# Kernel tuning notes

Hardware: AMD Instinct MI355X
Metric: run time of the kernel (lower is better)

## Reference

```python
import jax, jax.numpy as jnp
import numpy as np

D_MODEL = 1024
N_HEADS = 16
HEAD_DIM = D_MODEL // N_HEADS
SEQ_LEN = 2048
D_FF = 4 * D_MODEL
LCC_SCALE = 0.1
LN_EPS = 1e-5
NORM_EPS = 1e-12  # F.normalize eps


def _layer_norm(x, g, b):
    mu = jnp.mean(x, axis=-1, keepdims=True)
    var = jnp.mean(jnp.square(x - mu), axis=-1, keepdims=True)
    return (x - mu) * jax.lax.rsqrt(var + LN_EPS) * g + b


def setup_inputs() -> dict:
    key = jax.random.key(0)
    ks = jax.random.split(key, 8)
    s = 0.02  # weight init scale
    return {
        "x": jax.random.normal(ks[0], (SEQ_LEN, D_MODEL), jnp.float32),
        "lcc_values": jax.random.uniform(ks[1], (SEQ_LEN,), jnp.float32),
        "w_qkv": jax.random.normal(ks[2], (D_MODEL, 3 * D_MODEL), jnp.float32) * s,
        "b_qkv": jnp.zeros((3 * D_MODEL,), jnp.float32),
        "w_out": jax.random.normal(ks[3], (D_MODEL, D_MODEL), jnp.float32) * s,
        "b_out": jnp.zeros((D_MODEL,), jnp.float32),
        "ln1_g": jnp.ones((D_MODEL,), jnp.float32),
        "ln1_b": jnp.zeros((D_MODEL,), jnp.float32),
        "ln2_g": jnp.ones((D_MODEL,), jnp.float32),
        "ln2_b": jnp.zeros((D_MODEL,), jnp.float32),
        "w_ff1": jax.random.normal(ks[4], (D_MODEL, D_FF), jnp.float32) * s,
        "b_ff1": jnp.zeros((D_FF,), jnp.float32),
        "w_ff2": jax.random.normal(ks[5], (D_FF, D_MODEL), jnp.float32) * s,
        "b_ff2": jnp.zeros((D_MODEL,), jnp.float32),
    }


def reference(x, lcc_values, w_qkv, b_qkv, w_out, b_out, ln1_g, ln1_b,
              ln2_g, ln2_b, w_ff1, b_ff1, w_ff2, b_ff2):
    L = x.shape[0]
    scaling = HEAD_DIM ** -0.5

    normed = _layer_norm(x, ln1_g, ln1_b)
    qkv = normed @ w_qkv + b_qkv                      # [L, 3D]
    qkv = qkv.reshape(L, 3, N_HEADS, HEAD_DIM)
    q = jnp.transpose(qkv[:, 0], (1, 0, 2))           # [H, L, d]
    k = jnp.transpose(qkv[:, 1], (1, 0, 2))
    v = jnp.transpose(qkv[:, 2], (1, 0, 2))

    # cosine attention: L2-normalize q, k
    q = q / jnp.maximum(jnp.linalg.norm(q, axis=-1, keepdims=True), NORM_EPS)
    k = k / jnp.maximum(jnp.linalg.norm(k, axis=-1, keepdims=True), NORM_EPS)
    q = q * scaling

    scores = jnp.einsum('hld,hmd->hlm', q, k)         # [H, L, L]
    bias = (lcc_values[:, None] + lcc_values[None, :]) * 0.5 * LCC_SCALE
    scores = jnp.clip(scores + bias[None], -10.0, 10.0)
    probs = jax.nn.softmax(scores, axis=-1)

    attn = jnp.einsum('hlm,hmd->hld', probs, v)       # [H, L, d]
    attn = jnp.transpose(attn, (1, 0, 2)).reshape(L, D_MODEL)
    x = x + (attn @ w_out + b_out)

    normed2 = _layer_norm(x, ln2_g, ln2_b)
    h = jax.nn.gelu(normed2 @ w_ff1 + b_ff1, approximate=False)
    x = x + (h @ w_ff2 + b_ff2)
    return x
```

## Files before the change

### kernel.cpp

```cpp
#include <hip/hip_runtime.h>
#include <hip/hip_bf16.h>

#define D_MODEL 1024
#define SEQ 2048
#define NH 16
#define HD 64
#define DFF 4096

typedef __attribute__((ext_vector_type(8))) __bf16 bf16x8;
typedef __attribute__((ext_vector_type(4))) float f32x4;

__device__ __forceinline__ unsigned short f2bf(float f) {
    union { float f; unsigned u; } v; v.f = f;
    unsigned r = v.u + 0x7fffu + ((v.u >> 16) & 1u);
    return (unsigned short)(r >> 16);
}
__device__ __forceinline__ unsigned pack2(float a, float b) {
    return (unsigned)f2bf(a) | ((unsigned)f2bf(b) << 16);
}
__device__ __forceinline__ float bf2f(unsigned short u) {
    union { unsigned u; float f; } v; v.u = ((unsigned)u) << 16;
    return v.f;
}
__device__ __forceinline__ bf16x8 ld_frag(const unsigned short* p) {
    union { uint4 u; bf16x8 b; } c;
    c.u = *(const uint4*)p;
    return c.b;
}

typedef __attribute__((address_space(3))) unsigned lds_u32;
typedef const __attribute__((address_space(1))) unsigned glob_u32;
__device__ __forceinline__ void gl_lds16(const unsigned short* g, unsigned short* l) {
    __builtin_amdgcn_global_load_lds((glob_u32*)g, (lds_u32*)l, 16, 0, 0);
}

#define MFMA16(a,b,c) __builtin_amdgcn_mfma_f32_16x16x32_bf16(a,b,c,0,0,0)

__global__ __launch_bounds__(256) void wcast_all(const float* __restrict__ wq, const float* __restrict__ wo,
                                                 const float* __restrict__ wf1, const float* __restrict__ wf2,
                                                 unsigned short* __restrict__ oq, unsigned short* __restrict__ oo,
                                                 unsigned short* __restrict__ of1, unsigned short* __restrict__ of2) {
    __shared__ unsigned short lt[64][72];
    int id = blockIdx.x;
    const float* W; unsigned short* O; int K, N, nb, kb;
    if (id < 768)       { W = wq;  O = oq;  K = 1024; N = 3072; nb = id % 48; kb = id / 48; }
    else if (id < 1024) { id -= 768;  W = wo;  O = oo;  K = 1024; N = 1024; nb = id & 15; kb = id >> 4; }
    else if (id < 2048) { id -= 1024; W = wf1; O = of1; K = 1024; N = 4096; nb = id & 63; kb = id >> 6; }
    else                { id -= 2048; W = wf2; O = of2; K = 4096; N = 1024; nb = id & 15; kb = id >> 4; }
    int t = threadIdx.x;
    int r = t >> 2, c0 = (t & 3) << 4;
    const float* src = W + (size_t)(kb*64 + r) * N + nb*64 + c0;
    float4 f0 = ((const float4*)src)[0];
    float4 f1 = ((const float4*)src)[1];
    float4 f2 = ((const float4*)src)[2];
    float4 f3 = ((const float4*)src)[3];
    unsigned* dst = (unsigned*)&lt[r][c0];
    dst[0]=pack2(f0.x,f0.y); dst[1]=pack2(f0.z,f0.w);
    dst[2]=pack2(f1.x,f1.y); dst[3]=pack2(f1.z,f1.w);
    dst[4]=pack2(f2.x,f2.y); dst[5]=pack2(f2.z,f2.w);
    dst[6]=pack2(f3.x,f3.y); dst[7]=pack2(f3.z,f3.w);
    __syncthreads();
    int n_ = t >> 2, k0 = (t & 3) << 4;
    unsigned obuf[8];
#pragma unroll
    for (int i = 0; i < 8; i++)
        obuf[i] = (unsigned)lt[k0 + 2*i][n_] | ((unsigned)lt[k0 + 2*i + 1][n_] << 16);
    unsigned short* out = O + (size_t)(nb*64 + n_) * K + kb*64 + k0;
    ((uint4*)out)[0] = *(uint4*)&obuf[0];
    ((uint4*)out)[1] = *(uint4*)&obuf[4];
}

__global__ __launch_bounds__(256) void ln_kernel(const float* __restrict__ x,
                                                 const float* __restrict__ g,
                                                 const float* __restrict__ b,
                                                 unsigned short* __restrict__ out) {
    int row = blockIdx.x, t = threadIdx.x;
    float4 v = ((const float4*)(x + (size_t)row * D_MODEL))[t];
    float s  = v.x + v.y + v.z + v.w;
    float sq = v.x*v.x + v.y*v.y + v.z*v.z + v.w*v.w;
#pragma unroll
    for (int m = 1; m < 64; m <<= 1) { s += __shfl_xor(s, m, 64); sq += __shfl_xor(sq, m, 64); }
    __shared__ float ls[4], lq[4];
    int wave = t >> 6, lane = t & 63;
    if (lane == 0) { ls[wave] = s; lq[wave] = sq; }
    __syncthreads();
    s  = ls[0]+ls[1]+ls[2]+ls[3];
    sq = lq[0]+lq[1]+lq[2]+lq[3];
    float mu  = s * (1.0f / D_MODEL);
    float var = sq * (1.0f / D_MODEL) - mu * mu;
    float rs  = rsqrtf(var + 1e-5f);
    int c = t * 4;
    float y0 = (v.x - mu) * rs * g[c+0] + b[c+0];
    float y1 = (v.y - mu) * rs * g[c+1] + b[c+1];
    float y2 = (v.z - mu) * rs * g[c+2] + b[c+2];
    float y3 = (v.w - mu) * rs * g[c+3] + b[c+3];
    unsigned* o = (unsigned*)(out + (size_t)row * D_MODEL + c);
    o[0] = pack2(y0, y1); o[1] = pack2(y2, y3);
}

__global__ __launch_bounds__(256) void reduce_ln(const float* __restrict__ x,
                                                 const float* __restrict__ bout,
                                                 const unsigned short* __restrict__ parts,
                                                 const float* __restrict__ g,
                                                 const float* __restrict__ b,
                                                 float* __restrict__ x1,
                                                 unsigned short* __restrict__ x2n) {
    int row = blockIdx.x, t = threadIdx.x;
    int i = row * 256 + t;
    float4 v = ((const float4*)x)[i];
    float4 bb = ((const float4*)bout)[t];
    v.x += bb.x; v.y += bb.y; v.z += bb.z; v.w += bb.w;
    ushort4 u0 = ((const ushort4*)parts)[i];
    ushort4 u1 = ((const ushort4*)(parts + (size_t)SEQ*D_MODEL))[i];
    v.x += bf2f(u0.x) + bf2f(u1.x);
    v.y += bf2f(u0.y) + bf2f(u1.y);
    v.z += bf2f(u0.z) + bf2f(u1.z);
    v.w += bf2f(u0.w) + bf2f(u1.w);
    ((float4*)x1)[i] = v;
    float s  = v.x + v.y + v.z + v.w;
    float sq = v.x*v.x + v.y*v.y + v.z*v.z + v.w*v.w;
#pragma unroll
    for (int m = 1; m < 64; m <<= 1) { s += __shfl_xor(s, m, 64); sq += __shfl_xor(sq, m, 64); }
    __shared__ float ls[4], lq[4];
    int wave = t >> 6, lane = t & 63;
    if (lane == 0) { ls[wave] = s; lq[wave] = sq; }
    __syncthreads();
    s  = ls[0]+ls[1]+ls[2]+ls[3];
    sq = lq[0]+lq[1]+lq[2]+lq[3];
    float mu  = s * (1.0f / D_MODEL);
    float var = sq * (1.0f / D_MODEL) - mu * mu;
    float rs  = rsqrtf(var + 1e-5f);
    int c = t * 4;
    float y0 = (v.x - mu) * rs * g[c+0] + b[c+0];
    float y1 = (v.y - mu) * rs * g[c+1] + b[c+1];
    float y2 = (v.z - mu) * rs * g[c+2] + b[c+2];
    float y3 = (v.w - mu) * rs * g[c+3] + b[c+3];
    unsigned* o = (unsigned*)(x2n + (size_t)row * D_MODEL + c);
    o[0] = pack2(y0, y1); o[1] = pack2(y2, y3);
}

__global__ __launch_bounds__(256) void reduce_ff2(const float* __restrict__ res,
                                                  const float* __restrict__ bias,
                                                  const unsigned short* __restrict__ parts,
                                                  float* __restrict__ out) {
    int i = blockIdx.x * 256 + threadIdx.x;
    float4 r = ((const float4*)res)[i];
    float4 b = ((const float4*)bias)[i & (D_MODEL/4 - 1)];
    r.x += b.x; r.y += b.y; r.z += b.z; r.w += b.w;
#pragma unroll
    for (int p = 0; p < 4; p++) {
        ushort4 u = ((const ushort4*)(parts + (size_t)p * SEQ * D_MODEL))[i];
        r.x += bf2f(u.x); r.y += bf2f(u.y); r.z += bf2f(u.z); r.w += bf2f(u.w);
    }
    ((float4*)out)[i] = r;
}

#define TMg 128
#define TNg 64
#define SMEM_U16 (2 * (TMg + TNg) * 64)
__device__ __forceinline__ void gemm_core(const unsigned short* __restrict__ A,
                                          const unsigned short* __restrict__ Bt,
                                          int K, int K0, int KS, int bm, int bn,
                                          unsigned short* smem, f32x4 acc[4][2],
                                          int wave, int lane) {
    constexpr int AI = 4, BI = 2, MI = 4, NI = 2;
    constexpr int HALF = (TMg + TNg) * 64;
    int quad = lane >> 4, lr = lane & 15;

    const unsigned short* pa[AI];
    int aoff[AI];
#pragma unroll
    for (int i = 0; i < AI; i++) {
        int rl = wave*32 + i*8 + (lane >> 3);
        int ss = (lane & 7) ^ (rl & 7);
        pa[i] = A + (size_t)(bm*TMg + rl) * K + K0 + ss*8;
        aoff[i] = (wave*32 + i*8) * 64;
    }
    const unsigned short* pb[BI];
    int boff[BI];
#pragma unroll
    for (int i = 0; i < BI; i++) {
        int rl = wave*16 + i*8 + (lane >> 3);
        int ss = (lane & 7) ^ (rl & 7);
        pb[i] = Bt + (size_t)(bn*TNg + rl) * K + K0 + ss*8;
        boff[i] = TMg*64 + (wave*16 + i*8) * 64;
    }

    int wr = (wave >> 1) * 64, wc = (wave & 1) * 32;
    int foA[2][MI], foB[2][NI];
#pragma unroll
    for (int i = 0; i < MI; i++) {
        int row = wr + i*16 + lr;
        foA[0][i] = row*64 + ((quad     ^ (row & 7)))*8;
        foA[1][i] = row*64 + (((quad+4) ^ (row & 7)))*8;
    }
#pragma unroll
    for (int j = 0; j < NI; j++) {
        int row = wc + j*16 + lr;
        foB[0][j] = TMg*64 + row*64 + ((quad     ^ (row & 7)))*8;
        foB[1][j] = TMg*64 + row*64 + (((quad+4) ^ (row & 7)))*8;
    }

#pragma unroll
    for (int i = 0; i < AI; i++) gl_lds16(pa[i], smem + aoff[i]);
#pragma unroll
    for (int i = 0; i < BI; i++) gl_lds16(pb[i], smem + boff[i]);

    int bo = 0;
    for (int kk = 0; kk < KS; kk += 64) {
        __syncthreads();
        if (kk + 64 < KS) {
            int nb = bo ^ HALF;
#pragma unroll
            for (int i = 0; i < AI; i++) gl_lds16(pa[i] + kk + 64, smem + nb + aoff[i]);
#pragma unroll
            for (int i = 0; i < BI; i++) gl_lds16(pb[i] + kk + 64, smem + nb + boff[i]);
        }
#pragma unroll
        for (int h = 0; h < 2; h++) {
            bf16x8 af[MI], bfr[NI];
#pragma unroll
            for (int i = 0; i < MI; i++) af[i]  = ld_frag(smem + bo + foA[h][i]);
#pragma unroll
            for (int j = 0; j < NI; j++) bfr[j] = ld_frag(smem + bo + foB[h][j]);
#pragma unroll
            for (int i = 0; i < MI; i++)
#pragma unroll
                for (int j = 0; j < NI; j++)
                    acc[i][j] = MFMA16(af[i], bfr[j], acc[i][j]);
        }
        bo ^= HALF;
    }
}

__device__ __forceinline__ void acc_init(f32x4 acc[4][2]) {
    f32x4 z = {0.f, 0.f, 0.f, 0.f};
#pragma unroll
    for (int i = 0; i < 4; i++) { acc[i][0] = z; acc[i][1] = z; }
}

__global__ __launch_bounds__(256) void k_gemm_qkv(const unsigned short* __restrict__ A,
                                                  const unsigned short* __restrict__ Bt,
                                                  const float* __restrict__ bias,
                                                  unsigned short* __restrict__ qn,
                                                  unsigned short* __restrict__ kn,
                                                  unsigned short* __restrict__ vt) {
    __shared__ unsigned short smem[SMEM_U16];
    int t = threadIdx.x;
    int bn = blockIdx.x, bm = blockIdx.y;
    int wave = t >> 6, lane = t & 63;
    int quad = lane >> 4, lr = lane & 15;
    f32x4 acc[4][2];
    acc_init(acc);
    gemm_core(A, Bt, 1024, 0, 1024, bm, bn, smem, acc, wave, lane);

    int wr = (wave >> 1) * 64, wc = (wave & 1) * 32;
    int sec = bn >> 4, h = bn & 15;
    float bv0 = bias[bn*64 + wc + lr];
    float bv1 = bias[bn*64 + wc + 16 + lr];
#pragma unroll
    for (int i = 0; i < 4; i++)
#pragma unroll
        for (int r = 0; r < 4; r++) { acc[i][0][r] += bv0; acc[i][1][r] += bv1; }

    if (sec < 2) {
        float* sums = (float*)smem;
        __syncthreads();
#pragma unroll
        for (int i = 0; i < 4; i++)
#pragma unroll
            for (int r = 0; r < 4; r++) {
                float s = acc[i][0][r]*acc[i][0][r] + acc[i][1][r]*acc[i][1][r];
                s += __shfl_xor(s, 1, 64); s += __shfl_xor(s, 2, 64);
                s += __shfl_xor(s, 4, 64); s += __shfl_xor(s, 8, 64);
                if (lr == 0) sums[(wr + i*16 + quad*4 + r)*2 + (wave & 1)] = s;
            }
        __syncthreads();
        unsigned short* dst = (sec == 0) ? qn : kn;
        float mul = (sec == 0) ? 0.125f : 1.0f;
#pragma unroll
        for (int i = 0; i < 4; i++)
#pragma unroll
            for (int r = 0; r < 4; r++) {
                int row = wr + i*16 + quad*4 + r;
                float tot = sums[row*2] + sums[row*2 + 1];
                float scale = mul / fmaxf(sqrtf(tot), 1e-12f);
                size_t base = ((size_t)h*SEQ + bm*128 + row) * HD;
                dst[base + wc + lr]      = f2bf(acc[i][0][r] * scale);
                dst[base + wc + 16 + lr] = f2bf(acc[i][1][r] * scale);
            }
    } else {
        __syncthreads();
        unsigned short (*lv)[130] = (unsigned short (*)[130])smem;
#pragma unroll
        for (int i = 0; i < 4; i++)
#pragma unroll
            for (int j = 0; j < 2; j++)
#pragma unroll
                for (int r = 0; r < 4; r++)
                    lv[wc + j*16 + lr][wr + i*16 + quad*4 + r] = f2bf(acc[i][j][r]);
        __syncthreads();
        int d = t >> 2, l0 = (t & 3) * 32;
        unsigned short* ov = vt + ((size_t)(h*HD + d)) * SEQ + bm*128 + l0;
        ((uint4*)ov)[0] = *(uint4*)&lv[d][l0];
        ((uint4*)ov)[1] = *(uint4*)&lv[d][l0 + 8];
        ((uint4*)ov)[2] = *(uint4*)&lv[d][l0 + 16];
        ((uint4*)ov)[3] = *(uint4*)&lv[d][l0 + 24];
    }
}

template<int SPLITK>
__device__ __forceinline__ void gemm_part(const unsigned short* A, const unsigned short* Bt,
                                          unsigned short* C, int M, int N, int K) {
    __shared__ unsigned short smem[SMEM_U16];
    int t = threadIdx.x;
    int bn = blockIdx.x, bm = blockIdx.y, kz = blockIdx.z;
    int wave = t >> 6, lane = t & 63;
    int quad = lane >> 4, lr = lane & 15;
    int KS = K / SPLITK;
    f32x4 acc[4][2];
    acc_init(acc);
    gemm_core(A, Bt, K, kz*KS, KS, bm, bn, smem, acc, wave, lane);
    int wr = (wave >> 1) * 64, wc = (wave & 1) * 32;
    unsigned short* P = C + (size_t)kz * M * N;
#pragma unroll
    for (int i = 0; i < 4; i++)
#pragma unroll
        for (int j = 0; j < 2; j++) {
            int row0 = bm*TMg + wr + i*16 + quad*4;
            int col  = bn*TNg + wc + j*16 + lr;
#pragma unroll
            for (int r = 0; r < 4; r++)
                P[(size_t)(row0 + r) * N + col] = f2bf(acc[i][j][r]);
        }
}
__global__ __launch_bounds__(256) void k_gemm_op(const unsigned short* A, const unsigned short* Bt,
                                                 unsigned short* C, int M, int N, int K) {
    gemm_part<2>(A, Bt, C, M, N, K);
}
__global__ __launch_bounds__(256) void k_gemm_ff2(const unsigned short* A, const unsigned short* Bt,
                                                  unsigned short* C, int M, int N, int K) {
    gemm_part<4>(A, Bt, C, M, N, K);
}

__global__ __launch_bounds__(256) void k_gemm_ff1(const unsigned short* __restrict__ A,
                                                  const unsigned short* __restrict__ Bt,
                                                  const float* __restrict__ bias,
                                                  unsigned short* __restrict__ C,
                                                  int M, int N, int K) {
    __shared__ unsigned short smem[SMEM_U16];
    int t = threadIdx.x;
    int bn = blockIdx.x, bm = blockIdx.y;
    int wave = t >> 6, lane = t & 63;
    int quad = lane >> 4, lr = lane & 15;
    f32x4 acc[4][2];
    acc_init(acc);
    gemm_core(A, Bt, K, 0, K, bm, bn, smem, acc, wave, lane);
    int wr = (wave >> 1) * 64, wc = (wave & 1) * 32;
#pragma unroll
    for (int i = 0; i < 4; i++)
#pragma unroll
        for (int j = 0; j < 2; j++) {
            int row0 = bm*TMg + wr + i*16 + quad*4;
            int col  = bn*TNg + wc + j*16 + lr;
            float bv = bias[col];
#pragma unroll
            for (int r = 0; r < 4; r++) {
                float v = acc[i][j][r] + bv;
                v = 0.5f * v * (1.0f + erff(v * 0.70710678118654752f));
                C[(size_t)(row0 + r) * N + col] = f2bf(v);
            }
        }
}

#define KSPLIT 2
#define KTILES (SEQ / 64 / KSPLIT)
__global__ __launch_bounds__(256) void attn_kernel(const unsigned short* __restrict__ qn,
                                                   const unsigned short* __restrict__ kn,
                                                   const unsigned short* __restrict__ vt,
                                                   const float* __restrict__ lcc,
                                                   float* __restrict__ num_ws,
                                                   float* __restrict__ den_ws) {
    __shared__ unsigned short lQ[64][72];
    __shared__ unsigned short lK[64][72];
    __shared__ unsigned short lV[64][72];
    __shared__ unsigned short lP[64][72];
    __shared__ float lL[SEQ / KSPLIT];
    int h = blockIdx.x, qb = blockIdx.y, kz = blockIdx.z;
    int t = threadIdx.x;
    int rl = t >> 2, c0 = (t & 3) << 4;
    const unsigned short* pq = qn + ((size_t)h*SEQ + qb*64 + rl)*HD + c0;
    *(uint4*)&lQ[rl][c0]     = ((const uint4*)pq)[0];
    *(uint4*)&lQ[rl][c0 + 8] = ((const uint4*)pq)[1];
    for (int i = t; i < SEQ/KSPLIT; i += 256) lL[i] = 0.05f * lcc[kz*(SEQ/KSPLIT) + i];
    __syncthreads();
    int wave = t >> 6, lane = t & 63, quad = lane >> 4, lr = lane & 15;
    float lqv[4];
#pragma unroll
    for (int r = 0; r < 4; r++) lqv[r] = 0.05f * lcc[qb*64 + wave*16 + quad*4 + r];
    bf16x8 aq0 = ld_frag(&lQ[wave*16 + lr][quad*8]);
    bf16x8 aq1 = ld_frag(&lQ[wave*16 + lr][32 + quad*8]);
    f32x4 z = {0.f, 0.f, 0.f, 0.f};
    f32x4 oacc[4]; oacc[0]=z; oacc[1]=z; oacc[2]=z; oacc[3]=z;
    float den[4] = {0.f, 0.f, 0.f, 0.f};

    const unsigned short* kn0 = kn + (size_t)h*SEQ*HD + (size_t)kz*(SEQ/KSPLIT)*HD;
    const unsigned short* vt0 = vt + (size_t)h*HD*SEQ + kz*(SEQ/KSPLIT);

    for (int kb = 0; kb < KTILES; kb++) {
        __syncthreads();
        const unsigned short* pk = kn0 + (size_t)(kb*64 + rl)*HD + c0;
        uint4 k0v = ((const uint4*)pk)[0], k1v = ((const uint4*)pk)[1];
        const unsigned short* pv = vt0 + (size_t)rl*SEQ + kb*64 + c0;
        uint4 v0v = ((const uint4*)pv)[0], v1v = ((const uint4*)pv)[1];
        *(uint4*)&lK[rl][c0]     = k0v; *(uint4*)&lK[rl][c0 + 8] = k1v;
        *(uint4*)&lV[rl][c0]     = v0v; *(uint4*)&lV[rl][c0 + 8] = v1v;
        __syncthreads();
#pragma unroll
        for (int j = 0; j < 4; j++) {
            bf16x8 b0 = ld_frag(&lK[j*16 + lr][quad*8]);
            bf16x8 b1 = ld_frag(&lK[j*16 + lr][32 + quad*8]);
            f32x4 s = z;
            s = MFMA16(aq0, b0, s);
            s = MFMA16(aq1, b1, s);
            float lm = lL[kb*64 + j*16 + lr];
#pragma unroll
            for (int r = 0; r < 4; r++) {
                float sv = s[r] + lqv[r] + lm;
                sv = fminf(fmaxf(sv, -10.f), 10.f);
                float p = __expf(sv);
                den[r] += p;
                lP[wave*16 + quad*4 + r][j*16 + lr] = f2bf(p);
            }
        }
        bf16x8 ap0 = ld_frag(&lP[wave*16 + lr][quad*8]);
        bf16x8 ap1 = ld_frag(&lP[wave*16 + lr][32 + quad*8]);
#pragma unroll
        for (int j2 = 0; j2 < 4; j2++) {
            bf16x8 b0 = ld_frag(&lV[j2*16 + lr][quad*8]);
            bf16x8 b1 = ld_frag(&lV[j2*16 + lr][32 + quad*8]);
            oacc[j2] = MFMA16(ap0, b0, oacc[j2]);
            oacc[j2] = MFMA16(ap1, b1, oacc[j2]);
        }
    }
#pragma unroll
    for (int r = 0; r < 4; r++)
#pragma unroll
        for (int m = 1; m < 16; m <<= 1) den[r] += __shfl_xor(den[r], m, 64);

    float* nump = num_ws + (((size_t)(h*32 + qb)) * KSPLIT + kz) * 4096;
#pragma unroll
    for (int j2 = 0; j2 < 4; j2++)
#pragma unroll
        for (int r = 0; r < 4; r++)
            nump[(wave*16 + quad*4 + r) * 64 + j2*16 + lr] = oacc[j2][r];
    if (lr == 0) {
        float* denp = den_ws + (((size_t)(h*32 + qb)) * KSPLIT + kz) * 64;
#pragma unroll
        for (int r = 0; r < 4; r++) denp[wave*16 + quad*4 + r] = den[r];
    }
}

__global__ __launch_bounds__(256) void attn_comb(const float* __restrict__ num_ws,
                                                 const float* __restrict__ den_ws,
                                                 unsigned short* __restrict__ attn) {
    int hq = blockIdx.x;
    int h = hq >> 5, qb = hq & 31;
    int t = threadIdx.x;
    int row = t >> 2, col0 = (t & 3) << 4;
    const float* n0 = num_ws + ((size_t)hq * KSPLIT) * 4096 + row*64 + col0;
    const float* n1 = n0 + 4096;
    float d = den_ws[(size_t)hq * KSPLIT * 64 + row] + den_ws[((size_t)hq * KSPLIT + 1) * 64 + row];
    float inv = 1.0f / d;
    unsigned ob[8];
#pragma unroll
    for (int i = 0; i < 4; i++) {
        float4 a = ((const float4*)n0)[i];
        float4 b = ((const float4*)n1)[i];
        ob[2*i]   = pack2((a.x + b.x) * inv, (a.y + b.y) * inv);
        ob[2*i+1] = pack2((a.z + b.z) * inv, (a.w + b.w) * inv);
    }
    unsigned short* op = attn + (size_t)(qb*64 + row) * D_MODEL + h*64 + col0;
    ((uint4*)op)[0] = *(uint4*)&ob[0];
    ((uint4*)op)[1] = *(uint4*)&ob[4];
}

extern "C" void kernel_launch(void* const* d_in, const int* in_sizes, int n_in,
                              void* d_out, int out_size, void* d_ws, size_t ws_size,
                              hipStream_t stream) {
    const float* x      = (const float*)d_in[0];
    const float* lcc    = (const float*)d_in[1];
    const float* w_qkv  = (const float*)d_in[2];
    const float* b_qkv  = (const float*)d_in[3];
    const float* w_out  = (const float*)d_in[4];
    const float* b_out  = (const float*)d_in[5];
    const float* ln1_g  = (const float*)d_in[6];
    const float* ln1_b  = (const float*)d_in[7];
    const float* ln2_g  = (const float*)d_in[8];
    const float* ln2_b  = (const float*)d_in[9];
    const float* w_ff1  = (const float*)d_in[10];
    const float* b_ff1  = (const float*)d_in[11];
    const float* w_ff2  = (const float*)d_in[12];
    const float* b_ff2  = (const float*)d_in[13];

    char* ws = (char*)d_ws;
    unsigned short* wtq  = (unsigned short*)(ws);
    unsigned short* wto  = (unsigned short*)(ws + 6291456);
    unsigned short* wtf1 = (unsigned short*)(ws + 8388608);
    unsigned short* wtf2 = (unsigned short*)(ws + 16777216);
    unsigned short* xn   = (unsigned short*)(ws + 25165824);
    float*          x1   = (float*)(ws + 29360128);
    float*          numw = (float*)(ws + 29360128);
    float*          denw = (float*)(ws + 46137344);
    unsigned short* hbuf = (unsigned short*)(ws + 37748736);
    unsigned short* pOP  = (unsigned short*)(ws + 37748736);
    unsigned short* qnb  = (unsigned short*)(ws + 54525952);
    unsigned short* knb  = (unsigned short*)(ws + 58720256);
    unsigned short* vtb  = (unsigned short*)(ws + 62914560);
    unsigned short* pFF2 = (unsigned short*)(ws);
    unsigned short* attnb = xn;
    unsigned short* x2n  = qnb;
    float* outp = (float*)d_out;


    wcast_all<<<3072, 256, 0, stream>>>(w_qkv, w_out, w_ff1, w_ff2, wtq, wto, wtf1, wtf2);
    ln_kernel<<<SEQ, 256, 0, stream>>>(x, ln1_g, ln1_b, xn);
    k_gemm_qkv<<<dim3(48, 16), 256, 0, stream>>>(xn, wtq, b_qkv, qnb, knb, vtb);
    attn_kernel<<<dim3(16, 32, KSPLIT), 256, 0, stream>>>(qnb, knb, vtb, lcc, numw, denw);
    attn_comb<<<512, 256, 0, stream>>>(numw, denw, attnb);
    k_gemm_op<<<dim3(16, 16, 2), 256, 0, stream>>>(attnb, wto, pOP, SEQ, 1024, 1024);
    reduce_ln<<<SEQ, 256, 0, stream>>>(x, b_out, pOP, ln2_g, ln2_b, x1, x2n);
    k_gemm_ff1<<<dim3(64, 16), 256, 0, stream>>>(x2n, wtf1, b_ff1, hbuf, SEQ, 4096, 1024);
    k_gemm_ff2<<<dim3(16, 16, 4), 256, 0, stream>>>(hbuf, wtf2, pFF2, SEQ, 1024, 4096);
    reduce_ff2<<<SEQ*D_MODEL/1024, 256, 0, stream>>>(x1, b_ff2, pFF2, outp);
}
```

Baseline: 264.7 us.

## Widen GEMM block tile to 128x128 and compute q/k norms per-wave

All GEMMs now use 128x128 output tiles instead of 128x64. Each wave owns a 64x64 sub-tile, which doubles MFMA work per shared-memory fragment load and halves the grid sizes. In the QKV epilogue a wave's 64 columns now cover a full head, so the L2 norm is reduced with shuffles alone and the shared-memory exchange and two barriers go away. The costs are more accumulator registers, larger LDS use, and fewer blocks (for example 256 for the output projection), which may underfill the GPU.

```diff
diff --git a/kernel.cpp b/kernel.cpp
--- a/kernel.cpp
+++ b/kernel.cpp
@@ -156,14 +156,14 @@
 }
 
 #define TMg 128
-#define TNg 64
+#define TNg 128
 #define SMEM_U16 (2 * (TMg + TNg) * 64)
 __device__ __forceinline__ void gemm_core(const unsigned short* __restrict__ A,
                                           const unsigned short* __restrict__ Bt,
                                           int K, int K0, int KS, int bm, int bn,
-                                          unsigned short* smem, f32x4 acc[4][2],
+                                          unsigned short* smem, f32x4 acc[4][4],
                                           int wave, int lane) {
-    constexpr int AI = 4, BI = 2, MI = 4, NI = 2;
+    constexpr int AI = 4, BI = 4, MI = 4, NI = 4;
     constexpr int HALF = (TMg + TNg) * 64;
     int quad = lane >> 4, lr = lane & 15;
 
@@ -180,13 +180,13 @@
     int boff[BI];
 #pragma unroll
     for (int i = 0; i < BI; i++) {
-        int rl = wave*16 + i*8 + (lane >> 3);
+        int rl = wave*32 + i*8 + (lane >> 3);
         int ss = (lane & 7) ^ (rl & 7);
         pb[i] = Bt + (size_t)(bn*TNg + rl) * K + K0 + ss*8;
-        boff[i] = TMg*64 + (wave*16 + i*8) * 64;
-    }
-
-    int wr = (wave >> 1) * 64, wc = (wave & 1) * 32;
+        boff[i] = TMg*64 + (wave*32 + i*8) * 64;
+    }
+
+    int wr = (wave >> 1) * 64, wc = (wave & 1) * 64;
     int foA[2][MI], foB[2][NI];
 #pragma unroll
     for (int i = 0; i < MI; i++) {
@@ -233,10 +233,12 @@
     }
 }
 
-__device__ __forceinline__ void acc_init(f32x4 acc[4][2]) {
+__device__ __forceinline__ void acc_init(f32x4 acc[4][4]) {
     f32x4 z = {0.f, 0.f, 0.f, 0.f};
 #pragma unroll
-    for (int i = 0; i < 4; i++) { acc[i][0] = z; acc[i][1] = z; }
+    for (int i = 0; i < 4; i++)
+#pragma unroll
+        for (int j = 0; j < 4; j++) acc[i][j] = z;
 }
 
 __global__ __launch_bounds__(256) void k_gemm_qkv(const unsigned short* __restrict__ A,
@@ -250,62 +252,58 @@
     int bn = blockIdx.x, bm = blockIdx.y;
     int wave = t >> 6, lane = t & 63;
     int quad = lane >> 4, lr = lane & 15;
-    f32x4 acc[4][2];
+    f32x4 acc[4][4];
     acc_init(acc);
     gemm_core(A, Bt, 1024, 0, 1024, bm, bn, smem, acc, wave, lane);
 
-    int wr = (wave >> 1) * 64, wc = (wave & 1) * 32;
-    int sec = bn >> 4, h = bn & 15;
-    float bv0 = bias[bn*64 + wc + lr];
-    float bv1 = bias[bn*64 + wc + 16 + lr];
+    int wr = (wave >> 1) * 64, wc = (wave & 1) * 64;
+    int sec = bn >> 3, hp = bn & 7;
+    float bv[4];
+#pragma unroll
+    for (int j = 0; j < 4; j++) bv[j] = bias[bn*TNg + wc + j*16 + lr];
 #pragma unroll
     for (int i = 0; i < 4; i++)
 #pragma unroll
-        for (int r = 0; r < 4; r++) { acc[i][0][r] += bv0; acc[i][1][r] += bv1; }
+        for (int j = 0; j < 4; j++)
+#pragma unroll
+            for (int r = 0; r < 4; r++) acc[i][j][r] += bv[j];
 
     if (sec < 2) {
-        float* sums = (float*)smem;
-        __syncthreads();
-#pragma unroll
-        for (int i = 0; i < 4; i++)
-#pragma unroll
-            for (int r = 0; r < 4; r++) {
-                float s = acc[i][0][r]*acc[i][0][r] + acc[i][1][r]*acc[i][1][r];
-                s += __shfl_xor(s, 1, 64); s += __shfl_xor(s, 2, 64);
-                s += __shfl_xor(s, 4, 64); s += __shfl_xor(s, 8, 64);
-                if (lr == 0) sums[(wr + i*16 + quad*4 + r)*2 + (wave & 1)] = s;
-            }
-        __syncthreads();
+        int h = hp*2 + (wave & 1);
         unsigned short* dst = (sec == 0) ? qn : kn;
         float mul = (sec == 0) ? 0.125f : 1.0f;
 #pragma unroll
         for (int i = 0; i < 4; i++)
 #pragma unroll
             for (int r = 0; r < 4; r++) {
-                int row = wr + i*16 + quad*4 + r;
-                float tot = sums[row*2] + sums[row*2 + 1];
-                float scale = mul / fmaxf(sqrtf(tot), 1e-12f);
-                size_t base = ((size_t)h*SEQ + bm*128 + row) * HD;
-                dst[base + wc + lr]      = f2bf(acc[i][0][r] * scale);
-                dst[base + wc + 16 + lr] = f2bf(acc[i][1][r] * scale);
+                float ss = 0.f;
+#pragma unroll
+                for (int j = 0; j < 4; j++) ss += acc[i][j][r]*acc[i][j][r];
+                ss += __shfl_xor(ss, 1, 64); ss += __shfl_xor(ss, 2, 64);
+                ss += __shfl_xor(ss, 4, 64); ss += __shfl_xor(ss, 8, 64);
+                float scale = mul / fmaxf(sqrtf(ss), 1e-12f);
+                int row = bm*TMg + wr + i*16 + quad*4 + r;
+                size_t base = ((size_t)h*SEQ + row) * HD;
+#pragma unroll
+                for (int j = 0; j < 4; j++)
+                    dst[base + j*16 + lr] = f2bf(acc[i][j][r] * scale);
             }
     } else {
         __syncthreads();
-        unsigned short (*lv)[130] = (unsigned short (*)[130])smem;
+        unsigned short (*lv)[136] = (unsigned short (*)[136])smem;
 #pragma unroll
         for (int i = 0; i < 4; i++)
 #pragma unroll
-            for (int j = 0; j < 2; j++)
+            for (int j = 0; j < 4; j++)
 #pragma unroll
                 for (int r = 0; r < 4; r++)
                     lv[wc + j*16 + lr][wr + i*16 + quad*4 + r] = f2bf(acc[i][j][r]);
         __syncthreads();
-        int d = t >> 2, l0 = (t & 3) * 32;
-        unsigned short* ov = vt + ((size_t)(h*HD + d)) * SEQ + bm*128 + l0;
-        ((uint4*)ov)[0] = *(uint4*)&lv[d][l0];
-        ((uint4*)ov)[1] = *(uint4*)&lv[d][l0 + 8];
-        ((uint4*)ov)[2] = *(uint4*)&lv[d][l0 + 16];
-        ((uint4*)ov)[3] = *(uint4*)&lv[d][l0 + 24];
+        int d = t >> 1, l0 = (t & 1) * 64;
+        unsigned short* ov = vt + ((size_t)(hp*128 + d)) * SEQ + bm*TMg + l0;
+#pragma unroll
+        for (int c = 0; c < 8; c++)
+            ((uint4*)ov)[c] = *(uint4*)&lv[d][l0 + c*8];
     }
 }
 
@@ -318,15 +316,15 @@
     int wave = t >> 6, lane = t & 63;
     int quad = lane >> 4, lr = lane & 15;
     int KS = K / SPLITK;
-    f32x4 acc[4][2];
+    f32x4 acc[4][4];
     acc_init(acc);
     gemm_core(A, Bt, K, kz*KS, KS, bm, bn, smem, acc, wave, lane);
-    int wr = (wave >> 1) * 64, wc = (wave & 1) * 32;
+    int wr = (wave >> 1) * 64, wc = (wave & 1) * 64;
     unsigned short* P = C + (size_t)kz * M * N;
 #pragma unroll
     for (int i = 0; i < 4; i++)
 #pragma unroll
-        for (int j = 0; j < 2; j++) {
+        for (int j = 0; j < 4; j++) {
             int row0 = bm*TMg + wr + i*16 + quad*4;
             int col  = bn*TNg + wc + j*16 + lr;
 #pragma unroll
@@ -353,20 +351,20 @@
     int bn = blockIdx.x, bm = blockIdx.y;
     int wave = t >> 6, lane = t & 63;
     int quad = lane >> 4, lr = lane & 15;
-    f32x4 acc[4][2];
+    f32x4 acc[4][4];
     acc_init(acc);
     gemm_core(A, Bt, K, 0, K, bm, bn, smem, acc, wave, lane);
-    int wr = (wave >> 1) * 64, wc = (wave & 1) * 32;
+    int wr = (wave >> 1) * 64, wc = (wave & 1) * 64;
 #pragma unroll
     for (int i = 0; i < 4; i++)
 #pragma unroll
-        for (int j = 0; j < 2; j++) {
+        for (int j = 0; j < 4; j++) {
             int row0 = bm*TMg + wr + i*16 + quad*4;
             int col  = bn*TNg + wc + j*16 + lr;
-            float bv = bias[col];
+            float bvv = bias[col];
 #pragma unroll
             for (int r = 0; r < 4; r++) {
-                float v = acc[i][j][r] + bv;
+                float v = acc[i][j][r] + bvv;
                 v = 0.5f * v * (1.0f + erff(v * 0.70710678118654752f));
                 C[(size_t)(row0 + r) * N + col] = f2bf(v);
             }
@@ -525,12 +523,12 @@
 
     wcast_all<<<3072, 256, 0, stream>>>(w_qkv, w_out, w_ff1, w_ff2, wtq, wto, wtf1, wtf2);
     ln_kernel<<<SEQ, 256, 0, stream>>>(x, ln1_g, ln1_b, xn);
-    k_gemm_qkv<<<dim3(48, 16), 256, 0, stream>>>(xn, wtq, b_qkv, qnb, knb, vtb);
+    k_gemm_qkv<<<dim3(24, 16), 256, 0, stream>>>(xn, wtq, b_qkv, qnb, knb, vtb);
     attn_kernel<<<dim3(16, 32, KSPLIT), 256, 0, stream>>>(qnb, knb, vtb, lcc, numw, denw);
     attn_comb<<<512, 256, 0, stream>>>(numw, denw, attnb);
-    k_gemm_op<<<dim3(16, 16, 2), 256, 0, stream>>>(attnb, wto, pOP, SEQ, 1024, 1024);
+    k_gemm_op<<<dim3(8, 16, 2), 256, 0, stream>>>(attnb, wto, pOP, SEQ, 1024, 1024);
     reduce_ln<<<SEQ, 256, 0, stream>>>(x, b_out, pOP, ln2_g, ln2_b, x1, x2n);
-    k_gemm_ff1<<<dim3(64, 16), 256, 0, stream>>>(x2n, wtf1, b_ff1, hbuf, SEQ, 4096, 1024);
-    k_gemm_ff2<<<dim3(16, 16, 4), 256, 0, stream>>>(hbuf, wtf2, pFF2, SEQ, 1024, 4096);
+    k_gemm_ff1<<<dim3(32, 16), 256, 0, stream>>>(x2n, wtf1, b_ff1, hbuf, SEQ, 4096, 1024);
+    k_gemm_ff2<<<dim3(8, 16, 4), 256, 0, stream>>>(hbuf, wtf2, pFF2, SEQ, 1024, 4096);
     reduce_ff2<<<SEQ*D_MODEL/1024, 256, 0, stream>>>(x1, b_ff2, pFF2, outp);
 }
```

Measured after the change: 262.7 us. No clear change (-0.8%).
